# Kernel tuning notes

Measured on AMD Instinct MI355X. Metric: run time of the kernel, lower is better.

The kernel has to match this reference:

```python
import jax, jax.numpy as jnp
import numpy as np

TOP_K = 10
EPS = 1e-8


def setup_inputs() -> dict:
    key = jax.random.key(0)
    k1, k2, k3 = jax.random.split(key, 3)
    N, D = 8192, 1024
    return {
        "image_features": jax.random.normal(k1, (N, D), dtype=jnp.float32),
        "text_features": jax.random.normal(k2, (N, D), dtype=jnp.float32),
        "logit_scale": jnp.asarray(100.0, dtype=jnp.float32),
        "img_index": jax.random.randint(k3, (N,), 0, 1000, dtype=jnp.int64),
    }


def _soft_labels(text_features, img_index):
    # cosine similarity matrix (replaces the blocked double loop; same math)
    norms = jnp.linalg.norm(text_features, axis=1, keepdims=True)
    tn = text_features / jnp.maximum(norms, EPS)
    sim = tn @ tn.T                                  # (N, N)
    N = sim.shape[0]
    eye = jnp.eye(N, dtype=sim.dtype)
    # topk over sim with diagonal zeroed (matches fill_diagonal_(0) on a clone)
    k = min(TOP_K, N)
    _, idx = jax.lax.top_k(sim * (1.0 - eye), k)     # (N, k)
    rows = jnp.arange(N)[:, None]
    mask_sim = jnp.zeros_like(sim).at[rows, idx].set(1.0)
    mask_sim = jnp.where(eye > 0, 1.0, mask_sim)     # fill_diagonal_(1)
    mask_class = (img_index[:, None] == img_index[None, :]).astype(sim.dtype)
    s = sim * mask_sim * mask_class
    return s / jnp.sum(s, axis=1, keepdims=True)     # row-normalized soft labels


def reference(image_features, text_features, logit_scale, img_index):
    logits_per_image = logit_scale * (image_features @ text_features.T)
    logits_per_text = logit_scale * (text_features @ image_features.T)
    labels = _soft_labels(text_features, img_index)  # computed under no_grad in torch
    ce_i = jnp.mean(-jnp.sum(labels * jax.nn.log_softmax(logits_per_image, axis=-1), axis=-1))
    ce_t = jnp.mean(-jnp.sum(labels * jax.nn.log_softmax(logits_per_text, axis=-1), axis=-1))
    return (ce_i + ce_t) / 2
```

## Files before the change

kernel.cpp:

```cpp
#include <hip/hip_runtime.h>
#include <stdint.h>

#define N_ROWS 8192
#define D_DIM  1024
#define TOPK   10
#define NCLS   1000

typedef __attribute__((ext_vector_type(8))) short  s8v;
typedef __attribute__((ext_vector_type(4))) short  s4v;
typedef __attribute__((ext_vector_type(4))) float  f4v;
typedef __attribute__((ext_vector_type(4))) int    i4v;
typedef __attribute__((ext_vector_type(8))) int    i8v;
typedef unsigned long long u64;
typedef unsigned int       u32;
typedef unsigned char      u8;

static __device__ __forceinline__ short f2bf(float f) {
    union { float f; u32 u; } v; v.f = f;
    u32 u = v.u;
    u32 r = (u + 0x7fffu + ((u >> 16) & 1u)) >> 16;
    return (short)r;
}
static __device__ __forceinline__ float bf2f(short s) {
    union { float f; u32 u; } v;
    v.u = ((u32)(unsigned short)s) << 16;
    return v.f;
}

#if defined(__has_builtin)
#if __has_builtin(__builtin_amdgcn_cvt_pk_fp8_f32)
#define HAVE_CVT_FP8 1
#endif
#endif

static __device__ __forceinline__ u8 f2e4m3_sw(float x) {
    u32 u = __float_as_uint(x);
    u32 s = (u >> 24) & 0x80u;
    u32 a = u & 0x7fffffffu;
    if (a >= 0x43e00000u) return (u8)(s | 0x7e);
    if (a < 0x3c800000u) {
        float q = fabsf(x) * 512.0f;
        int n = (int)rintf(q);
        return (u8)(s | (u32)n);
    }
    u32 r = a + 0x0007ffffu + ((a >> 20) & 1u);
    u32 E = (r >> 23) - 127u + 7u;
    return (u8)(s | (E << 3) | ((r >> 20) & 7u));
}

static __device__ __forceinline__ u32 pack4_fp8(float f0, float f1, float f2, float f3) {
#ifdef HAVE_CVT_FP8
    u32 w = (u32)__builtin_amdgcn_cvt_pk_fp8_f32(f0, f1, 0, false);
    w = (u32)__builtin_amdgcn_cvt_pk_fp8_f32(f2, f3, (int)w, true);
    return w;
#else
    return (u32)f2e4m3_sw(f0) | ((u32)f2e4m3_sw(f1) << 8) |
           ((u32)f2e4m3_sw(f2) << 16) | ((u32)f2e4m3_sw(f3) << 24);
#endif
}

static __device__ __forceinline__ void BAR() {
    asm volatile("" ::: "memory");
    __builtin_amdgcn_s_barrier();
    asm volatile("" ::: "memory");
}
#define SBAR() __builtin_amdgcn_sched_barrier(0)

static __device__ __forceinline__ u64 packkey(float v, int idx) {
    u32 u = __float_as_uint(v);
    u = (u & 0x80000000u) ? ~u : (u | 0x80000000u);
    return ((u64)u << 32) | (u32)idx;
}

__global__ __launch_bounds__(256) void prep_kernel(
    const float* __restrict__ img, const float* __restrict__ txt,
    short* __restrict__ img_b, short* __restrict__ txt_b, short* __restrict__ tn_b,
    u32* __restrict__ img8, u32* __restrict__ txt8, u32* __restrict__ tn8)
{
    const int row = blockIdx.x;
    const int tid = threadIdx.x;
    const size_t base = (size_t)row * D_DIM + tid * 4;
    f4v tv = *(const f4v*)(txt + base);
    f4v iv = *(const f4v*)(img + base);
    float ss = tv[0]*tv[0] + tv[1]*tv[1] + tv[2]*tv[2] + tv[3]*tv[3];
    #pragma unroll
    for (int m = 32; m >= 1; m >>= 1) ss += __shfl_xor(ss, m);
    __shared__ float red4[4];
    if ((tid & 63) == 0) red4[tid >> 6] = ss;
    __syncthreads();
    float tot = red4[0] + red4[1] + red4[2] + red4[3];
    float inv = 1.0f / fmaxf(sqrtf(tot), 1e-8f);
    s4v tb, nb, ib;
    #pragma unroll
    for (int j = 0; j < 4; ++j) {
        tb[j] = f2bf(tv[j]);
        nb[j] = f2bf(tv[j] * inv);
        ib[j] = f2bf(iv[j]);
    }
    *(s4v*)(txt_b + base) = tb;
    *(s4v*)(tn_b  + base) = nb;
    *(s4v*)(img_b + base) = ib;
    const size_t wbase = (size_t)row * (D_DIM / 4) + tid;
    img8[wbase] = pack4_fp8(iv[0], iv[1], iv[2], iv[3]);
    txt8[wbase] = pack4_fp8(tv[0], tv[1], tv[2], tv[3]);
    tn8[wbase]  = pack4_fp8(tv[0]*inv, tv[1]*inv, tv[2]*inv, tv[3]*inv);
}

__global__ void detect_idx_kernel(const int* __restrict__ idx32, int* __restrict__ flag)
{
    int i = blockIdx.x * blockDim.x + threadIdx.x;
    if (idx32[2 * i + 1] != 0) atomicOr(flag, 1);
}

__global__ __launch_bounds__(256) void hist_kernel(const int* __restrict__ idx32,
    const int* __restrict__ flag, int* __restrict__ hist)
{
    const int i = blockIdx.x * 256 + threadIdx.x;
    const int is64 = (flag[0] == 0);
    const int c = is64 ? idx32[2 * i] : idx32[i];
    atomicAdd(&hist[c], 1);
}

__global__ void prefix_kernel(const int* __restrict__ hist, int* __restrict__ starts)
{
    const int lane = threadIdx.x;
    int acc = 0;
    for (int base = 0; base < NCLS; base += 64) {
        int v = (base + lane < NCLS) ? hist[base + lane] : 0;
        int p = v;
        #pragma unroll
        for (int s = 1; s < 64; s <<= 1) {
            int o = __shfl_up(p, s);
            if (lane >= s) p += o;
        }
        if (base + lane < NCLS) starts[base + lane] = acc + p - v;
        acc += __shfl(p, 63);
    }
    if (lane == 0) starts[NCLS] = acc;
}

__global__ __launch_bounds__(256) void scatter_kernel(const int* __restrict__ idx32,
    const int* __restrict__ flag, const int* __restrict__ starts,
    int* __restrict__ cursor, int* __restrict__ items)
{
    const int i = blockIdx.x * 256 + threadIdx.x;
    const int is64 = (flag[0] == 0);
    const int c = is64 ? idx32[2 * i] : idx32[i];
    const int pos = atomicAdd(&cursor[c], 1);
    items[starts[c] + pos] = i;
}

__device__ __forceinline__ void stageMX(u8* dstBuf, const u8* __restrict__ g,
                                        int grow0, int k0, int h, int tid)
{
    const int wid = tid >> 6;
    const int row = h * 64 + (tid >> 3);
    const int gch = (tid & 7) ^ ((tid >> 3) & 7);
    const u8* gp = g + (size_t)(grow0 + row) * D_DIM + k0 + gch * 16;
    u8* lp = dstBuf + h * 8192 + wid * 1024;
    __builtin_amdgcn_global_load_lds((const __attribute__((address_space(1))) void*)gp,
                                     (__attribute__((address_space(3))) void*)lp, 16, 0, 0);
}

static __device__ __forceinline__ i8v frag2(const u8* buf, int o0, int o1)
{
    i4v lo = *(const i4v*)(buf + o0);
    i4v hi = *(const i4v*)(buf + o1);
    return __builtin_shufflevector(lo, hi, 0, 1, 2, 3, 4, 5, 6, 7);
}

#define MFSC(m, n, af) \
    acc[m][n] = __builtin_amdgcn_mfma_scale_f32_16x16x128_f8f6f4( \
        af, bF[n], acc[m][n], 0, 0, 0, sc1, 0, sc1)

template<bool LAST>
__device__ __forceinline__ void kiterMX(int kt,
    const u8* __restrict__ A, const u8* __restrict__ B,
    int arow0, int brow0, int tid,
    const int* aof0, const int* aof1, const int* bof0, const int* bof1,
    const u8* curA, const u8* curB, u8* nxtA, u8* nxtB,
    f4v (&acc)[4][4], int sc1)
{
    const int k1 = (kt + 1) * 128;
    i8v aF0, aF1;
    i8v bF[4];
    aF0   = frag2(curA, aof0[0], aof1[0]);
    aF1   = frag2(curA, aof0[1], aof1[1]);
    bF[0] = frag2(curB, bof0[0], bof1[0]);
    bF[1] = frag2(curB, bof0[1], bof1[1]);
    if (!LAST) {
        stageMX(nxtA, A, arow0, k1, 0, tid);
        stageMX(nxtA, A, arow0, k1, 1, tid);
        stageMX(nxtB, B, brow0, k1, 0, tid);
        stageMX(nxtB, B, brow0, k1, 1, tid);
    }
    SBAR();
    __builtin_amdgcn_s_setprio(1);
    MFSC(0, 0, aF0); MFSC(0, 1, aF0); MFSC(1, 0, aF1); MFSC(1, 1, aF1);
    __builtin_amdgcn_s_setprio(0);
    SBAR();
    bF[2] = frag2(curB, bof0[2], bof1[2]);
    bF[3] = frag2(curB, bof0[3], bof1[3]);
    if (!LAST) {
        stageMX(nxtB, B, brow0, k1, 2, tid);
        stageMX(nxtB, B, brow0, k1, 3, tid);
    }
    SBAR();
    __builtin_amdgcn_s_setprio(1);
    MFSC(0, 2, aF0); MFSC(0, 3, aF0); MFSC(1, 2, aF1); MFSC(1, 3, aF1);
    __builtin_amdgcn_s_setprio(0);
    SBAR();
    aF0 = frag2(curA, aof0[2], aof1[2]);
    aF1 = frag2(curA, aof0[3], aof1[3]);
    SBAR();
    __builtin_amdgcn_s_setprio(1);
    MFSC(2, 2, aF0); MFSC(2, 3, aF0); MFSC(3, 2, aF1); MFSC(3, 3, aF1);
    __builtin_amdgcn_s_setprio(0);
    SBAR();
    __builtin_amdgcn_s_setprio(1);
    MFSC(2, 0, aF0); MFSC(2, 1, aF0); MFSC(3, 0, aF1); MFSC(3, 1, aF1);
    __builtin_amdgcn_s_setprio(0);
    if (!LAST) {
        asm volatile("s_waitcnt vmcnt(0)" ::: "memory");
        SBAR();
    }
    BAR();
}

__global__ __launch_bounds__(512, 2) void gemm_both(
    const u8* __restrict__ tn8, const u8* __restrict__ img8,
    const u8* __restrict__ txt8,
    float* __restrict__ partTop,
    u64* __restrict__ rowKeys, u64* __restrict__ colKeys)
{
    __shared__ u8 sA[2][16384];
    __shared__ u8 sB[2][32768];

    const int tid   = threadIdx.x;
    const int lane  = tid & 63, wid = tid >> 6;
    const int wr    = wid >> 2, wc = wid & 3;
    const int rlane = lane & 15, klane = lane >> 4;
    const int sc1   = 0x7f7f7f7f;

    const int bid  = blockIdx.x;
    const int mode = (bid >= 1056) ? 1 : 0;
    int rb, cb;
    if (mode == 0) {
        const int t = (bid & 7) * 132 + (bid >> 3);
        int c = (int)((sqrtf(4.0f * (float)t + 1.0f) - 1.0f) * 0.5f);
        while ((c + 1) * (c + 2) <= t) ++c;
        while (c * (c + 1) > t) --c;
        cb = c; rb = t - c * (c + 1);
    } else {
        const int b2 = bid - 1056;
        const int x = b2 & 7, q = b2 >> 3;
        const int chunk = q >> 6, inner = q & 63;
        rb = x * 8 + (inner & 7);
        cb = chunk * 8 + (inner >> 3);
    }
    const u8* A = mode ? img8 : tn8;
    const u8* B = mode ? txt8 : tn8;
    const int arow0 = rb * 128, brow0 = cb * 256;

    int aof0[4], aof1[4], bof0[4], bof1[4];
    #pragma unroll
    for (int f = 0; f < 4; ++f) {
        const int ra = wr * 64 + f * 16 + rlane;
        const int c0 = (klane * 2) ^ (ra & 7);
        aof0[f] = ra * 128 + c0 * 16;
        aof1[f] = ra * 128 + (((klane * 2 + 1)) ^ (ra & 7)) * 16;
        const int rbw = wc * 64 + f * 16 + rlane;
        const int d0 = (klane * 2) ^ (rbw & 7);
        bof0[f] = rbw * 128 + d0 * 16;
        bof1[f] = rbw * 128 + (((klane * 2 + 1)) ^ (rbw & 7)) * 16;
    }

    f4v acc[4][4];
    #pragma unroll
    for (int m = 0; m < 4; ++m)
        #pragma unroll
        for (int n = 0; n < 4; ++n)
            acc[m][n] = (f4v){0.f, 0.f, 0.f, 0.f};

    stageMX(&sA[0][0], A, arow0, 0, 0, tid);
    stageMX(&sA[0][0], A, arow0, 0, 1, tid);
    #pragma unroll
    for (int h = 0; h < 4; ++h) stageMX(&sB[0][0], B, brow0, 0, h, tid);
    asm volatile("s_waitcnt vmcnt(0)" ::: "memory");
    SBAR();
    BAR();

    #pragma unroll 1
    for (int kt2 = 0; kt2 < 3; ++kt2) {
        kiterMX<false>(2 * kt2,     A, B, arow0, brow0, tid, aof0, aof1, bof0, bof1,
                       &sA[0][0], &sB[0][0], &sA[1][0], &sB[1][0], acc, sc1);
        kiterMX<false>(2 * kt2 + 1, A, B, arow0, brow0, tid, aof0, aof1, bof0, bof1,
                       &sA[1][0], &sB[1][0], &sA[0][0], &sB[0][0], acc, sc1);
    }
    kiterMX<false>(6, A, B, arow0, brow0, tid, aof0, aof1, bof0, bof1,
                   &sA[0][0], &sB[0][0], &sA[1][0], &sB[1][0], acc, sc1);
    kiterMX<true>(7, A, B, arow0, brow0, tid, aof0, aof1, bof0, bof1,
                  &sA[1][0], &sB[1][0], &sA[0][0], &sB[0][0], acc, sc1);
    __syncthreads();

    if (mode == 1) {
        #pragma unroll
        for (int m = 0; m < 4; ++m) {
            #pragma unroll
            for (int rr = 0; rr < 4; ++rr) {
                float bv = acc[m][0][rr]; int bn = 0;
                #pragma unroll
                for (int n = 1; n < 4; ++n)
                    if (acc[m][n][rr] > bv) { bv = acc[m][n][rr]; bn = n; }
                u64 key = packkey(bv, cb * 256 + wc * 64 + bn * 16 + rlane);
                #pragma unroll
                for (int s = 1; s < 16; s <<= 1) {
                    u64 o = __shfl_xor(key, s);
                    if (o > key) key = o;
                }
                const u64 k1 = key;
                const int wcol = (int)(u32)k1;
                float bv2 = -INFINITY; int bn2 = 0;
                #pragma unroll
                for (int n = 0; n < 4; ++n) {
                    int gc = cb * 256 + wc * 64 + n * 16 + rlane;
                    if (gc != wcol && acc[m][n][rr] > bv2) { bv2 = acc[m][n][rr]; bn2 = n; }
                }
                u64 key2 = packkey(bv2, cb * 256 + wc * 64 + bn2 * 16 + rlane);
                if ((cb * 256 + wc * 64 + bn2 * 16 + rlane) == wcol) key2 = 0;
                #pragma unroll
                for (int s = 1; s < 16; s <<= 1) {
                    u64 o = __shfl_xor(key2, s);
                    if (o > key2) key2 = o;
                }
                if (rlane == 0) {
                    const int grow = rb * 128 + wr * 64 + m * 16 + klane * 4 + rr;
                    u64* dst = rowKeys + ((size_t)grow * 128 + cb * 4 + wc) * 2;
                    dst[0] = k1; dst[1] = key2;
                }
            }
        }
        #pragma unroll
        for (int n = 0; n < 4; ++n) {
            float bv = -INFINITY; int bi = 0;
            #pragma unroll
            for (int m = 0; m < 4; ++m)
                #pragma unroll
                for (int rr = 0; rr < 4; ++rr)
                    if (acc[m][n][rr] > bv) { bv = acc[m][n][rr]; bi = m * 16 + klane * 4 + rr; }
            u64 key = packkey(bv, rb * 128 + wr * 64 + bi);
            { u64 o = __shfl_xor(key, 16); if (o > key) key = o; }
            { u64 o = __shfl_xor(key, 32); if (o > key) key = o; }
            const u64 k1 = key;
            const int wrow = (int)(u32)k1;
            float bv2 = -INFINITY; int bi2 = -1;
            #pragma unroll
            for (int m = 0; m < 4; ++m)
                #pragma unroll
                for (int rr = 0; rr < 4; ++rr) {
                    int gr = rb * 128 + wr * 64 + m * 16 + klane * 4 + rr;
                    if (gr != wrow && acc[m][n][rr] > bv2) { bv2 = acc[m][n][rr]; bi2 = gr; }
                }
            u64 key2 = (bi2 >= 0) ? packkey(bv2, bi2) : 0;
            { u64 o = __shfl_xor(key2, 16); if (o > key2) key2 = o; }
            { u64 o = __shfl_xor(key2, 32); if (o > key2) key2 = o; }
            if (klane == 0) {
                const int gcol = cb * 256 + wc * 64 + n * 16 + rlane;
                u64* dst = colKeys + ((size_t)gcol * 128 + rb * 2 + wr) * 2;
                dst[0] = k1; dst[1] = key2;
            }
        }
    } else {
        #pragma unroll
        for (int m = 0; m < 4; ++m) {
            #pragma unroll
            for (int rr = 0; rr < 4; ++rr) {
                const int grow = rb * 128 + wr * 64 + m * 16 + klane * 4 + rr;
                float v[4];
                #pragma unroll
                for (int n = 0; n < 4; ++n) {
                    v[n] = acc[m][n][rr];
                    const int gcol = cb * 256 + wc * 64 + n * 16 + rlane;
                    if (gcol == grow) v[n] = 0.0f;
                }
                float t3[3];
                #pragma unroll
                for (int rd = 0; rd < 3; ++rd) {
                    float lm = fmaxf(fmaxf(v[0], v[1]), fmaxf(v[2], v[3]));
                    #pragma unroll
                    for (int s = 1; s < 16; s <<= 1) lm = fmaxf(lm, __shfl_xor(lm, s));
                    t3[rd] = lm;
                    #pragma unroll
                    for (int n = 0; n < 4; ++n) v[n] = (v[n] == lm) ? -INFINITY : v[n];
                }
                if (rlane == 0) {
                    float* dst = partTop + (size_t)grow * 384 + (size_t)(cb * 4 + wc) * 3;
                    dst[0] = t3[0]; dst[1] = t3[1]; dst[2] = t3[2];
                }
            }
        }
        #pragma unroll
        for (int n = 0; n < 4; ++n) {
            const int gcol = cb * 256 + wc * 64 + n * 16 + rlane;
            float vv[16];
            #pragma unroll
            for (int m = 0; m < 4; ++m)
                #pragma unroll
                for (int rr = 0; rr < 4; ++rr) {
                    const int grow = rb * 128 + wr * 64 + m * 16 + klane * 4 + rr;
                    float val = acc[m][n][rr];
                    if (grow == gcol) val = 0.0f;
                    vv[m * 4 + rr] = val;
                }
            float w0 = -INFINITY, w1 = -INFINITY, w2 = -INFINITY;
            #pragma unroll
            for (int rd = 0; rd < 3; ++rd) {
                float lm = vv[0];
                #pragma unroll
                for (int q = 1; q < 16; ++q) lm = fmaxf(lm, vv[q]);
                if (rd == 0) w0 = lm; else if (rd == 1) w1 = lm; else w2 = lm;
                #pragma unroll
                for (int q = 0; q < 16; ++q) vv[q] = (vv[q] == lm) ? -INFINITY : vv[q];
            }
            #pragma unroll
            for (int s = 16; s < 64; s <<= 1) {
                float o0 = __shfl_xor(w0, s), o1 = __shfl_xor(w1, s), o2 = __shfl_xor(w2, s);
                float c6[6] = {w0, w1, w2, o0, o1, o2};
                #pragma unroll
                for (int rd = 0; rd < 3; ++rd) {
                    float lm = c6[0];
                    #pragma unroll
                    for (int q = 1; q < 6; ++q) lm = fmaxf(lm, c6[q]);
                    if (rd == 0) w0 = lm; else if (rd == 1) w1 = lm; else w2 = lm;
                    #pragma unroll
                    for (int q = 0; q < 6; ++q) c6[q] = (c6[q] == lm) ? -INFINITY : c6[q];
                }
            }
            if (klane == 0) {
                float* dst = partTop + (size_t)gcol * 384 + (size_t)(rb * 2 + wr) * 3;
                dst[0] = w0; dst[1] = w1; dst[2] = w2;
            }
        }
    }
}

__global__ __launch_bounds__(256) void finalize_kernel(
    const short* __restrict__ img_b, const short* __restrict__ txt_b,
    const short* __restrict__ tn_b,
    const float* __restrict__ scale_p,
    const int* __restrict__ idx32, const int* __restrict__ flag,
    const int* __restrict__ starts, const int* __restrict__ items,
    const float* __restrict__ partTop,
    const u64* __restrict__ rowKeys, const u64* __restrict__ colKeys,
    float* __restrict__ contrib)
{
    const int i   = blockIdx.x;
    const int tid = threadIdx.x;
    const int lane = tid & 63, w = tid >> 6;
    __shared__ float s_thr;
    __shared__ int   s_rc[4], s_cc[4];
    __shared__ float ldots[8];
    __shared__ int   s_candN;
    __shared__ int   s_cj[16];
    __shared__ float s_cv[16];
    __shared__ int   sel[20];
    __shared__ float selw[20];
    __shared__ int   s_cnt;
    __shared__ float s_dots[20];

    if (tid == 0) s_candN = 0;

    if (w == 0) {
        const float* p = partTop + (size_t)i * 384 + lane * 6;
        float v[6];
        #pragma unroll
        for (int q = 0; q < 6; ++q) v[q] = p[q];
        float best = -INFINITY;
        #pragma unroll
        for (int r = 0; r < TOPK; ++r) {
            best = v[0];
            #pragma unroll
            for (int q = 1; q < 6; ++q) best = fmaxf(best, v[q]);
            #pragma unroll
            for (int m = 1; m < 64; m <<= 1) best = fmaxf(best, __shfl_xor(best, m));
            #pragma unroll
            for (int q = 0; q < 6; ++q) v[q] = (v[q] == best) ? -INFINITY : v[q];
        }
        if (lane == 0) s_thr = best;
    } else if (w == 1 || w == 2) {
        const u64* p = (w == 1) ? rowKeys + (size_t)i * 256 + lane * 4
                                : colKeys + (size_t)i * 256 + lane * 4;
        int* out = (w == 1) ? s_rc : s_cc;
        u64 k[4];
        #pragma unroll
        for (int q = 0; q < 4; ++q) k[q] = p[q];
        int chosen[4];
        #pragma unroll
        for (int r = 0; r < 4; ++r) {
            u64 best = 0;
            #pragma unroll
            for (int q = 0; q < 4; ++q) {
                int c = (int)(u32)k[q];
                bool excl = false;
                for (int e = 0; e < r; ++e) excl |= (c == chosen[e]);
                if (!excl && k[q] > best) best = k[q];
            }
            #pragma unroll
            for (int s = 1; s < 64; s <<= 1) {
                u64 o = __shfl_xor(best, s);
                if (o > best) best = o;
            }
            chosen[r] = (int)(u32)best;
        }
        if (lane == 0) {
            #pragma unroll
            for (int r = 0; r < 4; ++r) out[r] = chosen[r];
        }
    }
    __syncthreads();

    {
        const int is64 = (flag[0] == 0);
        const int ci = is64 ? idx32[2 * i] : idx32[i];
        const int s0 = starts[ci], s1 = starts[ci + 1];
        const float t = s_thr - 1e-5f;
        const short* ai = tn_b + (size_t)i * D_DIM + lane * 16;
        s8v a0 = *(const s8v*)ai, a1 = *(const s8v*)(ai + 8);
        for (int q = s0 + w; q < s1; q += 4) {
            const int j = items[q];
            if (j == i) continue;
            const short* bj = tn_b + (size_t)j * D_DIM + lane * 16;
            s8v b0 = *(const s8v*)bj, b1 = *(const s8v*)(bj + 8);
            float s = 0.f;
            #pragma unroll
            for (int e = 0; e < 8; ++e)
                s += bf2f(a0[e]) * bf2f(b0[e]) + bf2f(a1[e]) * bf2f(b1[e]);
            #pragma unroll
            for (int m = 1; m < 64; m <<= 1) s += __shfl_xor(s, m);
            if (lane == 0 && s >= t) {
                int pos = atomicAdd(&s_candN, 1);
                if (pos < 16) { s_cj[pos] = j; s_cv[pos] = s; }
            }
        }
    }
    __syncthreads();

    if (tid == 0) {
        int c = 1; sel[0] = i; selw[0] = 1.0f;
        const int nc = s_candN < 16 ? s_candN : 16;
        for (int q = 0; q < nc && c < 20; ++q) { sel[c] = s_cj[q]; selw[c] = s_cv[q]; ++c; }
        for (int a = 2; a < c; ++a) {
            int ky = sel[a]; float kv = selw[a]; int b = a - 1;
            while (b >= 1 && sel[b] > ky) { sel[b + 1] = sel[b]; selw[b + 1] = selw[b]; --b; }
            sel[b + 1] = ky; selw[b + 1] = kv;
        }
        s_cnt = c;
    }
    __syncthreads();

    const int c = s_cnt;
    for (int jj = w; jj < 8 + c; jj += 4) {
        int j; const short *ap, *bp;
        bool dual = false;
        if (jj < 4)      { j = s_rc[jj];      ap = img_b + (size_t)i * D_DIM; bp = txt_b + (size_t)j * D_DIM; }
        else if (jj < 8) { j = s_cc[jj - 4];  ap = txt_b + (size_t)i * D_DIM; bp = img_b + (size_t)j * D_DIM; }
        else             { j = sel[jj - 8];   ap = img_b + (size_t)i * D_DIM; bp = txt_b + (size_t)j * D_DIM; dual = true; }
        const short* ap2 = txt_b + (size_t)i * D_DIM + lane * 16;
        const short* bp2 = img_b + (size_t)j * D_DIM + lane * 16;
        ap += lane * 16; bp += lane * 16;
        s8v a0 = *(const s8v*)ap, a1 = *(const s8v*)(ap + 8);
        s8v b0 = *(const s8v*)bp, b1 = *(const s8v*)(bp + 8);
        float s = 0.f;
        #pragma unroll
        for (int e = 0; e < 8; ++e)
            s += bf2f(a0[e]) * bf2f(b0[e]) + bf2f(a1[e]) * bf2f(b1[e]);
        if (dual) {
            s8v c0 = *(const s8v*)ap2, c1 = *(const s8v*)(ap2 + 8);
            s8v d0 = *(const s8v*)bp2, d1 = *(const s8v*)(bp2 + 8);
            #pragma unroll
            for (int e = 0; e < 8; ++e)
                s += bf2f(c0[e]) * bf2f(d0[e]) + bf2f(c1[e]) * bf2f(d1[e]);
        }
        #pragma unroll
        for (int m = 1; m < 64; m <<= 1) s += __shfl_xor(s, m);
        if (lane == 0) {
            if (jj < 8) ldots[jj] = s;
            else        s_dots[jj - 8] = s;
        }
    }
    __syncthreads();

    if (tid == 0) {
        const float sc = scale_p[0];
        float rm = fmaxf(fmaxf(ldots[0], ldots[1]), fmaxf(ldots[2], ldots[3]));
        float rs = 0.f;
        #pragma unroll
        for (int q = 0; q < 4; ++q) rs += __expf(sc * (ldots[q] - rm));
        float rlse = sc * rm + __logf(rs);
        float cm = fmaxf(fmaxf(ldots[4], ldots[5]), fmaxf(ldots[6], ldots[7]));
        float cs = 0.f;
        #pragma unroll
        for (int q = 4; q < 8; ++q) cs += __expf(sc * (ldots[q] - cm));
        float clse = sc * cm + __logf(cs);
        float den = 0.f;
        for (int s = 0; s < c; ++s) den += selw[s];
        float acc = 0.f;
        for (int s = 0; s < c; ++s) acc += (selw[s] / den) * sc * s_dots[s];
        contrib[i] = rlse + clse - acc;
    }
}

__global__ __launch_bounds__(256) void reduce_kernel(
    const float* __restrict__ contrib, float* __restrict__ out)
{
    const int tid = threadIdx.x;
    float s = 0.f;
    for (int i = tid; i < N_ROWS; i += 256) s += contrib[i];
    #pragma unroll
    for (int m = 32; m >= 1; m >>= 1) s += __shfl_xor(s, m);
    __shared__ float r4[4];
    if ((tid & 63) == 0) r4[tid >> 6] = s;
    __syncthreads();
    if (tid == 0) out[0] = (r4[0] + r4[1] + r4[2] + r4[3]) * (0.5f / (float)N_ROWS);
}

extern "C" void kernel_launch(void* const* d_in, const int* in_sizes, int n_in,
                              void* d_out, int out_size, void* d_ws, size_t ws_size,
                              hipStream_t stream)
{
    const float* img     = (const float*)d_in[0];
    const float* txt     = (const float*)d_in[1];
    const float* scale_p = (const float*)d_in[2];
    const int*   idx32   = (const int*)d_in[3];

    char* ws = (char*)d_ws;
    short* img_b   = (short*)ws; ws += (size_t)N_ROWS * D_DIM * 2;
    short* txt_b   = (short*)ws; ws += (size_t)N_ROWS * D_DIM * 2;
    short* tn_b    = (short*)ws; ws += (size_t)N_ROWS * D_DIM * 2;
    u32*   img8    = (u32*)ws;   ws += (size_t)N_ROWS * D_DIM;
    u32*   txt8    = (u32*)ws;   ws += (size_t)N_ROWS * D_DIM;
    u32*   tn8     = (u32*)ws;   ws += (size_t)N_ROWS * D_DIM;
    float* partTop = (float*)ws; ws += (size_t)N_ROWS * 384 * 4;
    u64*   rowKeys = (u64*)ws;   ws += (size_t)N_ROWS * 256 * 8;
    u64*   colKeys = (u64*)ws;   ws += (size_t)N_ROWS * 256 * 8;
    float* contrib = (float*)ws; ws += N_ROWS * 4;
    int*   hist    = (int*)ws;   ws += 4096;
    int*   starts  = (int*)ws;   ws += 4096;
    int*   cursor  = (int*)ws;   ws += 4096;
    int*   items   = (int*)ws;   ws += N_ROWS * 4;
    int*   flag    = (int*)ws;   ws += 256;
    float* outf    = (float*)d_out;

    hipMemsetAsync(flag, 0, sizeof(int), stream);
    hipMemsetAsync(hist, 0, NCLS * sizeof(int), stream);
    hipMemsetAsync(cursor, 0, NCLS * sizeof(int), stream);

    prep_kernel<<<N_ROWS, 256, 0, stream>>>(img, txt, img_b, txt_b, tn_b,
                                            img8, txt8, tn8);
    detect_idx_kernel<<<16, 256, 0, stream>>>(idx32, flag);
    hist_kernel<<<N_ROWS / 256, 256, 0, stream>>>(idx32, flag, hist);
    prefix_kernel<<<1, 64, 0, stream>>>(hist, starts);
    scatter_kernel<<<N_ROWS / 256, 256, 0, stream>>>(idx32, flag, starts, cursor, items);
    gemm_both<<<3104, 512, 0, stream>>>((const u8*)tn8, (const u8*)img8,
                                        (const u8*)txt8, partTop, rowKeys, colKeys);
    finalize_kernel<<<N_ROWS, 256, 0, stream>>>(img_b, txt_b, tn_b, scale_p,
                                                idx32, flag, starts, items,
                                                partTop, rowKeys, colKeys, contrib);
    reduce_kernel<<<1, 256, 0, stream>>>(contrib, outf);
}
```

Before: 354.9 us.

## Triple-buffer LDS staging in the MX GEMM k-loop for deeper prefetch

Converts the double-buffered LDS pipeline into a triple-buffered one that prefetches two k-tiles ahead. Each iteration waits with vmcnt(6) instead of draining all loads, which keeps one stage of global-to-LDS copies in flight. The k-loop is fully unrolled, with a dedicated drain step for the final tiles. This raises LDS use per block from 96 KB to 144 KB, which can cut occupancy from two blocks per CU to one.

After: 357.0 us. About the same (+0.6%).

```diff
diff --git a/kernel.cpp b/kernel.cpp
--- a/kernel.cpp
+++ b/kernel.cpp
@@ -173,26 +173,25 @@
     acc[m][n] = __builtin_amdgcn_mfma_scale_f32_16x16x128_f8f6f4( \
         af, bF[n], acc[m][n], 0, 0, 0, sc1, 0, sc1)
 
-template<bool LAST>
-__device__ __forceinline__ void kiterMX(int kt,
+template<int DRAIN>
+__device__ __forceinline__ void kiterMX(
     const u8* __restrict__ A, const u8* __restrict__ B,
-    int arow0, int brow0, int tid,
+    int arow0, int brow0, int k2, int tid,
     const int* aof0, const int* aof1, const int* bof0, const int* bof1,
     const u8* curA, const u8* curB, u8* nxtA, u8* nxtB,
     f4v (&acc)[4][4], int sc1)
 {
-    const int k1 = (kt + 1) * 128;
     i8v aF0, aF1;
     i8v bF[4];
     aF0   = frag2(curA, aof0[0], aof1[0]);
     aF1   = frag2(curA, aof0[1], aof1[1]);
     bF[0] = frag2(curB, bof0[0], bof1[0]);
     bF[1] = frag2(curB, bof0[1], bof1[1]);
-    if (!LAST) {
-        stageMX(nxtA, A, arow0, k1, 0, tid);
-        stageMX(nxtA, A, arow0, k1, 1, tid);
-        stageMX(nxtB, B, brow0, k1, 0, tid);
-        stageMX(nxtB, B, brow0, k1, 1, tid);
+    if (DRAIN == 6) {
+        stageMX(nxtA, A, arow0, k2, 0, tid);
+        stageMX(nxtA, A, arow0, k2, 1, tid);
+        stageMX(nxtB, B, brow0, k2, 0, tid);
+        stageMX(nxtB, B, brow0, k2, 1, tid);
     }
     SBAR();
     __builtin_amdgcn_s_setprio(1);
@@ -201,9 +200,9 @@
     SBAR();
     bF[2] = frag2(curB, bof0[2], bof1[2]);
     bF[3] = frag2(curB, bof0[3], bof1[3]);
-    if (!LAST) {
-        stageMX(nxtB, B, brow0, k1, 2, tid);
-        stageMX(nxtB, B, brow0, k1, 3, tid);
+    if (DRAIN == 6) {
+        stageMX(nxtB, B, brow0, k2, 2, tid);
+        stageMX(nxtB, B, brow0, k2, 3, tid);
     }
     SBAR();
     __builtin_amdgcn_s_setprio(1);
@@ -220,11 +219,15 @@
     __builtin_amdgcn_s_setprio(1);
     MFSC(2, 0, aF0); MFSC(2, 1, aF0); MFSC(3, 0, aF1); MFSC(3, 1, aF1);
     __builtin_amdgcn_s_setprio(0);
-    if (!LAST) {
+    if (DRAIN == 6) {
+        asm volatile("s_waitcnt vmcnt(6)" ::: "memory");
+        SBAR();
+        BAR();
+    } else if (DRAIN == 0) {
         asm volatile("s_waitcnt vmcnt(0)" ::: "memory");
         SBAR();
-    }
-    BAR();
+        BAR();
+    }
 }
 
 __global__ __launch_bounds__(512, 2) void gemm_both(
@@ -233,8 +236,8 @@
     float* __restrict__ partTop,
     u64* __restrict__ rowKeys, u64* __restrict__ colKeys)
 {
-    __shared__ u8 sA[2][16384];
-    __shared__ u8 sB[2][32768];
+    __shared__ u8 sA[3][16384];
+    __shared__ u8 sB[3][32768];
 
     const int tid   = threadIdx.x;
     const int lane  = tid & 63, wid = tid >> 6;
@@ -266,12 +269,10 @@
     #pragma unroll
     for (int f = 0; f < 4; ++f) {
         const int ra = wr * 64 + f * 16 + rlane;
-        const int c0 = (klane * 2) ^ (ra & 7);
-        aof0[f] = ra * 128 + c0 * 16;
+        aof0[f] = ra * 128 + (((klane * 2))     ^ (ra & 7)) * 16;
         aof1[f] = ra * 128 + (((klane * 2 + 1)) ^ (ra & 7)) * 16;
         const int rbw = wc * 64 + f * 16 + rlane;
-        const int d0 = (klane * 2) ^ (rbw & 7);
-        bof0[f] = rbw * 128 + d0 * 16;
+        bof0[f] = rbw * 128 + (((klane * 2))     ^ (rbw & 7)) * 16;
         bof1[f] = rbw * 128 + (((klane * 2 + 1)) ^ (rbw & 7)) * 16;
     }
 
@@ -286,21 +287,30 @@
     stageMX(&sA[0][0], A, arow0, 0, 1, tid);
     #pragma unroll
     for (int h = 0; h < 4; ++h) stageMX(&sB[0][0], B, brow0, 0, h, tid);
-    asm volatile("s_waitcnt vmcnt(0)" ::: "memory");
+    stageMX(&sA[1][0], A, arow0, 128, 0, tid);
+    stageMX(&sA[1][0], A, arow0, 128, 1, tid);
+    #pragma unroll
+    for (int h = 0; h < 4; ++h) stageMX(&sB[1][0], B, brow0, 128, h, tid);
+    asm volatile("s_waitcnt vmcnt(6)" ::: "memory");
     SBAR();
     BAR();
 
-    #pragma unroll 1
-    for (int kt2 = 0; kt2 < 3; ++kt2) {
-        kiterMX<false>(2 * kt2,     A, B, arow0, brow0, tid, aof0, aof1, bof0, bof1,
-                       &sA[0][0], &sB[0][0], &sA[1][0], &sB[1][0], acc, sc1);
-        kiterMX<false>(2 * kt2 + 1, A, B, arow0, brow0, tid, aof0, aof1, bof0, bof1,
-                       &sA[1][0], &sB[1][0], &sA[0][0], &sB[0][0], acc, sc1);
-    }
-    kiterMX<false>(6, A, B, arow0, brow0, tid, aof0, aof1, bof0, bof1,
-                   &sA[0][0], &sB[0][0], &sA[1][0], &sB[1][0], acc, sc1);
-    kiterMX<true>(7, A, B, arow0, brow0, tid, aof0, aof1, bof0, bof1,
-                  &sA[1][0], &sB[1][0], &sA[0][0], &sB[0][0], acc, sc1);
+    kiterMX<6>(A, B, arow0, brow0, 2 * 128, tid, aof0, aof1, bof0, bof1,
+               &sA[0][0], &sB[0][0], &sA[2][0], &sB[2][0], acc, sc1);
+    kiterMX<6>(A, B, arow0, brow0, 3 * 128, tid, aof0, aof1, bof0, bof1,
+               &sA[1][0], &sB[1][0], &sA[0][0], &sB[0][0], acc, sc1);
+    kiterMX<6>(A, B, arow0, brow0, 4 * 128, tid, aof0, aof1, bof0, bof1,
+               &sA[2][0], &sB[2][0], &sA[1][0], &sB[1][0], acc, sc1);
+    kiterMX<6>(A, B, arow0, brow0, 5 * 128, tid, aof0, aof1, bof0, bof1,
+               &sA[0][0], &sB[0][0], &sA[2][0], &sB[2][0], acc, sc1);
+    kiterMX<6>(A, B, arow0, brow0, 6 * 128, tid, aof0, aof1, bof0, bof1,
+               &sA[1][0], &sB[1][0], &sA[0][0], &sB[0][0], acc, sc1);
+    kiterMX<6>(A, B, arow0, brow0, 7 * 128, tid, aof0, aof1, bof0, bof1,
+               &sA[2][0], &sB[2][0], &sA[1][0], &sB[1][0], acc, sc1);
+    kiterMX<0>(A, B, arow0, brow0, 0, tid, aof0, aof1, bof0, bof1,
+               &sA[0][0], &sB[0][0], nullptr, nullptr, acc, sc1);
+    kiterMX<-1>(A, B, arow0, brow0, 0, tid, aof0, aof1, bof0, bof1,
+                &sA[1][0], &sB[1][0], nullptr, nullptr, acc, sc1);
     __syncthreads();
 
     if (mode == 1) {
```
